# Optimization experiments

Measured on AMD Instinct MI355X. Metric: run time of the kernel, lower is better.

The kernel has to match this reference:

```python
import jax, jax.numpy as jnp
import numpy as np

B, S, K, D = 128, 64, 10, 256
THR = -1.5


def setup_inputs() -> dict:
    key = jax.random.key(0)
    ks = jax.random.split(key, 9)
    si = 1.0 / np.sqrt(D)  # torch GRU init: U(-1/sqrt(hidden), 1/sqrt(hidden))
    u = lambda k, shape, s: jax.random.uniform(k, shape, jnp.float32, -s, s)
    return {
        "item_embs": jax.random.normal(ks[0], (B, S, K, D), jnp.float32),
        "user_embs": jax.random.normal(ks[1], (B, S, D), jnp.float32),
        "W_ih": u(ks[2], (3 * D, 2 * D), si),
        "W_hh": u(ks[3], (3 * D, D), si),
        "b_ih": u(ks[4], (3 * D,), si),
        "b_hh": u(ks[5], (3 * D,), si),
        "w_out": u(ks[6], (D,), si),
        "b_out": u(ks[7], (), si),
        "length": jax.random.randint(ks[8], (B,), 0, S),
    }


def reference(item_embs, user_embs, W_ih, W_hh, b_ih, b_hh, w_out, b_out, length):
    N = B * S
    # x['items'] = cat([item_embs.flatten(0,1), zeros_like(...)], -1)  -> [N, K, 2D]
    items_flat = item_embs.reshape(N, K, D)
    items = jnp.concatenate([items_flat, jnp.zeros_like(items_flat)], axis=-1)
    # user hidden state: gather user_embs at (length-1, clamped), repeat over S
    idx = jnp.clip(length - 1, 0, None)  # [B]
    u0 = user_embs[jnp.arange(B), idx]   # [B, D]
    h0 = jnp.repeat(u0, S, axis=0)       # [N, D]

    def gru_cell(x, h):
        gi = x @ W_ih.T + b_ih  # [N, 3D]
        gh = h @ W_hh.T + b_hh
        i_r, i_z, i_n = jnp.split(gi, 3, axis=-1)
        h_r, h_z, h_n = jnp.split(gh, 3, axis=-1)
        r = jax.nn.sigmoid(i_r + h_r)
        z = jax.nn.sigmoid(i_z + h_z)
        n = jnp.tanh(i_n + r * h_n)
        return (1.0 - z) * n + z * h

    def step(carry, x_t):
        h, mask = carry  # mask [N,1]: readout threshold gate for the click-half of input
        x = jnp.concatenate([x_t[:, :D], x_t[:, D:] * mask], axis=-1)
        h = gru_cell(x, h)
        y = h @ w_out + b_out  # [N]
        next_mask = (jax.lax.stop_gradient(y) > THR).astype(x_t.dtype)[:, None]
        return (h, next_mask), y

    xs = jnp.swapaxes(items, 0, 1)  # [K, N, 2D]
    init = (h0, jnp.ones((N, 1), item_embs.dtype))
    _, ys = jax.lax.scan(step, init, xs)  # ys [K, N]
    y = jnp.swapaxes(ys, 0, 1)  # [N, K]
    # self.w = 1, self.b = 0 -> identity calibration
    return y.reshape(B, S, K)
```

## Files before the change

kernel.cpp:

```cpp
#include <hip/hip_runtime.h>

#define BB 128
#define SS 64
#define KK 10
#define DD 256
#define NN (BB*SS)
#define ROWS 32
#define NBLK (NN/ROWS)
#define NT 1024

typedef __attribute__((ext_vector_type(8))) short short8;
typedef __attribute__((ext_vector_type(4))) float f32x4;

#define FRAG_ELEMS (48*8*64*8)

__device__ __forceinline__ unsigned short f2bf(float f){
  union { float f; unsigned u; } v; v.f = f;
  unsigned r = (v.u + 0x7FFFu + ((v.u >> 16) & 1u)) >> 16;
  return (unsigned short)r;
}

__global__ void prep_weights(const float* __restrict__ Wih,
                             const float* __restrict__ Whh,
                             unsigned short* __restrict__ fw){
  int id = blockIdx.x * 256 + threadIdx.x;
  int arr = (id >= FRAG_ELEMS);
  int r = arr ? (id - FRAG_ELEMS) : id;
  int j  = r & 7;
  int l  = (r >> 3) & 63;
  int tk = (r >> 9) & 7;
  int tn = r >> 12;
  int c  = tn * 16 + (l & 15);
  int d  = tk * 32 + ((l >> 4) << 3) + j;
  float v = arr ? Whh[c * 256 + d] : Wih[c * 512 + d];
  fw[id] = f2bf(v);
}

__global__ __launch_bounds__(NT, 4) void gru_main(
    const float* __restrict__ item, const float* __restrict__ user,
    const float* __restrict__ b_ih, const float* __restrict__ b_hh,
    const float* __restrict__ w_out, const float* __restrict__ b_out,
    const int* __restrict__ length, const unsigned short* __restrict__ ws,
    float* __restrict__ out)
{
  __shared__ unsigned short xfrag[2][2*8*64*8];
  __shared__ unsigned short hfrag[2][2*8*64*8];
  __shared__ float yp[3][16][2][4][4];

  const int tid  = threadIdx.x;
  const int lane = tid & 63;
  const int w    = tid >> 6;
  const int col  = lane & 15;
  const int q    = lane >> 4;
  const int nb   = blockIdx.x * ROWS;
  const int b    = nb / SS;

  const short8* fw1 = (const short8*)ws;
  const short8* fwh = fw1 + (FRAG_ELEMS/8);

  const int d    = w*16 + col;
  const float br_  = b_ih[d]       + b_hh[d];
  const float bz_  = b_ih[256 + d] + b_hh[256 + d];
  const float bin_ = b_ih[512 + d];
  const float bhn_ = b_hh[512 + d];
  const float wo_  = w_out[d];

  int idx = length[b] - 1; if (idx < 0) idx = 0;
  const float u0 = user[((size_t)b*SS + idx)*DD + d];
  float h[2][4];
  #pragma unroll
  for (int mt = 0; mt < 2; ++mt)
    #pragma unroll
    for (int reg = 0; reg < 4; ++reg)
      h[mt][reg] = u0;

  const int tkk = d >> 5;
  const int slb = ((d >> 3) & 3) * 16;
  const int dj  = d & 7;
  {
    unsigned short hb = f2bf(u0);
    #pragma unroll
    for (int mt = 0; mt < 2; ++mt)
      #pragma unroll
      for (int reg = 0; reg < 4; ++reg)
        hfrag[0][((mt*8 + tkk)*64 + slb + q*4 + reg)*8 + dj] = hb;
  }

  const int xrow = tid >> 5;
  const int xo   = tid & 31;
  const int xmt  = xrow >> 4;
  const int xtk  = xo >> 2;
  const int xsl  = (xo & 3)*16 + (xrow & 15);
  {
    const float4* p = (const float4*)(item + ((size_t)(nb + xrow)*KK + 0)*DD + xo*8);
    float4 a0 = p[0], a1 = p[1];
    unsigned short t[8];
    t[0]=f2bf(a0.x); t[1]=f2bf(a0.y); t[2]=f2bf(a0.z); t[3]=f2bf(a0.w);
    t[4]=f2bf(a1.x); t[5]=f2bf(a1.y); t[6]=f2bf(a1.z); t[7]=f2bf(a1.w);
    *(short8*)&xfrag[0][((xmt*8 + xtk)*64 + xsl)*8] = *(short8*)t;
  }
  __syncthreads();

  const float bout = b_out[0];

  for (int k = 0; k < KK; ++k){
    const int cb  = k & 1;
    const int nbf = cb ^ 1;

    f32x4 acc[2][4];
    #pragma unroll
    for (int mt = 0; mt < 2; ++mt)
      #pragma unroll
      for (int kd = 0; kd < 4; ++kd){
        f32x4 z4 = {0.f, 0.f, 0.f, 0.f};
        acc[mt][kd] = z4;
      }

    #pragma unroll 2
    for (int tk = 0; tk < 8; ++tk){
      short8 ax0 = *(const short8*)&xfrag[cb][((0*8 + tk)*64 + lane)*8];
      short8 ax1 = *(const short8*)&xfrag[cb][((1*8 + tk)*64 + lane)*8];
      short8 ah0 = *(const short8*)&hfrag[cb][((0*8 + tk)*64 + lane)*8];
      short8 ah1 = *(const short8*)&hfrag[cb][((1*8 + tk)*64 + lane)*8];
      short8 w1r = fw1[((w     )*8 + tk)*64 + lane];
      short8 w1z = fw1[((16 + w)*8 + tk)*64 + lane];
      short8 w1n = fw1[((32 + w)*8 + tk)*64 + lane];
      short8 whr = fwh[((w     )*8 + tk)*64 + lane];
      short8 whz = fwh[((16 + w)*8 + tk)*64 + lane];
      short8 whn = fwh[((32 + w)*8 + tk)*64 + lane];
      acc[0][0] = __builtin_amdgcn_mfma_f32_16x16x32_bf16(ax0, w1r, acc[0][0], 0, 0, 0);
      acc[0][0] = __builtin_amdgcn_mfma_f32_16x16x32_bf16(ah0, whr, acc[0][0], 0, 0, 0);
      acc[0][1] = __builtin_amdgcn_mfma_f32_16x16x32_bf16(ax0, w1z, acc[0][1], 0, 0, 0);
      acc[0][1] = __builtin_amdgcn_mfma_f32_16x16x32_bf16(ah0, whz, acc[0][1], 0, 0, 0);
      acc[0][2] = __builtin_amdgcn_mfma_f32_16x16x32_bf16(ax0, w1n, acc[0][2], 0, 0, 0);
      acc[0][3] = __builtin_amdgcn_mfma_f32_16x16x32_bf16(ah0, whn, acc[0][3], 0, 0, 0);
      acc[1][0] = __builtin_amdgcn_mfma_f32_16x16x32_bf16(ax1, w1r, acc[1][0], 0, 0, 0);
      acc[1][0] = __builtin_amdgcn_mfma_f32_16x16x32_bf16(ah1, whr, acc[1][0], 0, 0, 0);
      acc[1][1] = __builtin_amdgcn_mfma_f32_16x16x32_bf16(ax1, w1z, acc[1][1], 0, 0, 0);
      acc[1][1] = __builtin_amdgcn_mfma_f32_16x16x32_bf16(ah1, whz, acc[1][1], 0, 0, 0);
      acc[1][2] = __builtin_amdgcn_mfma_f32_16x16x32_bf16(ax1, w1n, acc[1][2], 0, 0, 0);
      acc[1][3] = __builtin_amdgcn_mfma_f32_16x16x32_bf16(ah1, whn, acc[1][3], 0, 0, 0);
    }

    float4 xn0, xn1;
    if (k < KK-1){
      const float4* p = (const float4*)(item + ((size_t)(nb + xrow)*KK + (k+1))*DD + xo*8);
      xn0 = p[0]; xn1 = p[1];
    }

    float ypl[2][4];
    #pragma unroll
    for (int mt = 0; mt < 2; ++mt)
      #pragma unroll
      for (int reg = 0; reg < 4; ++reg){
        float rp = acc[mt][0][reg] + br_;
        float zp = acc[mt][1][reg] + bz_;
        float r  = 1.f / (1.f + __expf(-rp));
        float z  = 1.f / (1.f + __expf(-zp));
        float np = acc[mt][2][reg] + bin_ + r*(acc[mt][3][reg] + bhn_);
        np = fminf(fmaxf(np, -30.f), 30.f);
        float e  = __expf(2.f*np);
        float n  = (e - 1.f) / (e + 1.f);
        float hv = (1.f - z)*n + z*h[mt][reg];
        h[mt][reg] = hv;
        ypl[mt][reg] = hv * wo_;
      }

    #pragma unroll
    for (int mt = 0; mt < 2; ++mt)
      #pragma unroll
      for (int reg = 0; reg < 4; ++reg){
        float p = ypl[mt][reg];
        p += __shfl_xor(p, 1);
        p += __shfl_xor(p, 2);
        p += __shfl_xor(p, 4);
        p += __shfl_xor(p, 8);
        if (col == 0) yp[k % 3][w][mt][q][reg] = p;
      }

    #pragma unroll
    for (int mt = 0; mt < 2; ++mt)
      #pragma unroll
      for (int reg = 0; reg < 4; ++reg)
        hfrag[nbf][((mt*8 + tkk)*64 + slb + q*4 + reg)*8 + dj] = f2bf(h[mt][reg]);

    if (k < KK-1){
      unsigned short t[8];
      t[0]=f2bf(xn0.x); t[1]=f2bf(xn0.y); t[2]=f2bf(xn0.z); t[3]=f2bf(xn0.w);
      t[4]=f2bf(xn1.x); t[5]=f2bf(xn1.y); t[6]=f2bf(xn1.z); t[7]=f2bf(xn1.w);
      *(short8*)&xfrag[nbf][((xmt*8 + xtk)*64 + xsl)*8] = *(short8*)t;
    }

    if (k > 0 && tid < 32){
      float s = bout;
      #pragma unroll
      for (int ww = 0; ww < 16; ++ww)
        s += yp[(k-1) % 3][ww][tid >> 4][(tid >> 2) & 3][tid & 3];
      out[(size_t)(nb + tid)*KK + (k-1)] = s;
    }

    __syncthreads();
  }

  if (tid < 32){
    float s = bout;
    #pragma unroll
    for (int ww = 0; ww < 16; ++ww)
      s += yp[(KK-1) % 3][ww][tid >> 4][(tid >> 2) & 3][tid & 3];
    out[(size_t)(nb + tid)*KK + (KK-1)] = s;
  }
}

extern "C" void kernel_launch(void* const* d_in, const int* in_sizes, int n_in,
                              void* d_out, int out_size, void* d_ws, size_t ws_size,
                              hipStream_t stream) {
  const float* item   = (const float*)d_in[0];
  const float* user   = (const float*)d_in[1];
  const float* W_ih   = (const float*)d_in[2];
  const float* W_hh   = (const float*)d_in[3];
  const float* b_ih   = (const float*)d_in[4];
  const float* b_hh   = (const float*)d_in[5];
  const float* w_out  = (const float*)d_in[6];
  const float* b_out  = (const float*)d_in[7];
  const int*   length = (const int*)d_in[8];
  unsigned short* ws  = (unsigned short*)d_ws;
  float* out = (float*)d_out;

  hipLaunchKernelGGL(prep_weights, dim3((2*FRAG_ELEMS)/256), dim3(256), 0, stream,
                     W_ih, W_hh, ws);
  hipLaunchKernelGGL(gru_main, dim3(NBLK), dim3(NT), 0, stream,
                     item, user, b_ih, b_hh, w_out, b_out, length, ws, out);
}
```

Before: 232.7 us.

## Software-pipeline weight fragment loads with block-staggered K order and fast gate math

```diff
diff --git a/kernel.cpp b/kernel.cpp
--- a/kernel.cpp
+++ b/kernel.cpp
@@ -54,6 +54,7 @@
   const int q    = lane >> 4;
   const int nb   = blockIdx.x * ROWS;
   const int b    = nb / SS;
+  const int sk   = blockIdx.x & 7;
 
   const short8* fw1 = (const short8*)ws;
   const short8* fwh = fw1 + (FRAG_ELEMS/8);
@@ -64,6 +65,10 @@
   const float bin_ = b_ih[512 + d];
   const float bhn_ = b_hh[512 + d];
   const float wo_  = w_out[d];
+
+  const int wq0 = (w     )*512 + lane;
+  const int wq1 = (16 + w)*512 + lane;
+  const int wq2 = (32 + w)*512 + lane;
 
   int idx = length[b] - 1; if (idx < 0) idx = 0;
   const float u0 = user[((size_t)b*SS + idx)*DD + d];
@@ -99,9 +104,34 @@
     t[4]=f2bf(a1.x); t[5]=f2bf(a1.y); t[6]=f2bf(a1.z); t[7]=f2bf(a1.w);
     *(short8*)&xfrag[0][((xmt*8 + xtk)*64 + xsl)*8] = *(short8*)t;
   }
+
+  short8 wa0,wa1,wa2,wa3,wa4,wa5, wb0,wb1,wb2,wb3,wb4,wb5;
+  {
+    const int o_ = sk*64;
+    wa0 = fw1[wq0+o_]; wa1 = fw1[wq1+o_]; wa2 = fw1[wq2+o_];
+    wa3 = fwh[wq0+o_]; wa4 = fwh[wq1+o_]; wa5 = fwh[wq2+o_];
+  }
+
   __syncthreads();
 
   const float bout = b_out[0];
+
+#define MFMA16(A,Bv,C) __builtin_amdgcn_mfma_f32_16x16x32_bf16(A,Bv,C,0,0,0)
+#define TKSTEP(C0,C1,C2,C3,C4,C5, N0,N1,N2,N3,N4,N5, TK) do{ \
+      const int tkv_ = ((TK)+sk)&7; const int o_ = (((TK)+1+sk)&7)*64; \
+      N0 = fw1[wq0+o_]; N1 = fw1[wq1+o_]; N2 = fw1[wq2+o_]; \
+      N3 = fwh[wq0+o_]; N4 = fwh[wq1+o_]; N5 = fwh[wq2+o_]; \
+      short8 ax0 = *(const short8*)&xfrag[cb][((    tkv_)*64 + lane)*8]; \
+      short8 ax1 = *(const short8*)&xfrag[cb][((8 + tkv_)*64 + lane)*8]; \
+      short8 ah0 = *(const short8*)&hfrag[cb][((    tkv_)*64 + lane)*8]; \
+      short8 ah1 = *(const short8*)&hfrag[cb][((8 + tkv_)*64 + lane)*8]; \
+      acc[0][0] = MFMA16(ax0,C0,acc[0][0]); acc[0][0] = MFMA16(ah0,C3,acc[0][0]); \
+      acc[0][1] = MFMA16(ax0,C1,acc[0][1]); acc[0][1] = MFMA16(ah0,C4,acc[0][1]); \
+      acc[0][2] = MFMA16(ax0,C2,acc[0][2]); acc[0][3] = MFMA16(ah0,C5,acc[0][3]); \
+      acc[1][0] = MFMA16(ax1,C0,acc[1][0]); acc[1][0] = MFMA16(ah1,C3,acc[1][0]); \
+      acc[1][1] = MFMA16(ax1,C1,acc[1][1]); acc[1][1] = MFMA16(ah1,C4,acc[1][1]); \
+      acc[1][2] = MFMA16(ax1,C2,acc[1][2]); acc[1][3] = MFMA16(ah1,C5,acc[1][3]); \
+    }while(0)
 
   for (int k = 0; k < KK; ++k){
     const int cb  = k & 1;
@@ -115,32 +145,6 @@
         f32x4 z4 = {0.f, 0.f, 0.f, 0.f};
         acc[mt][kd] = z4;
       }
-
-    #pragma unroll 2
-    for (int tk = 0; tk < 8; ++tk){
-      short8 ax0 = *(const short8*)&xfrag[cb][((0*8 + tk)*64 + lane)*8];
-      short8 ax1 = *(const short8*)&xfrag[cb][((1*8 + tk)*64 + lane)*8];
-      short8 ah0 = *(const short8*)&hfrag[cb][((0*8 + tk)*64 + lane)*8];
-      short8 ah1 = *(const short8*)&hfrag[cb][((1*8 + tk)*64 + lane)*8];
-      short8 w1r = fw1[((w     )*8 + tk)*64 + lane];
-      short8 w1z = fw1[((16 + w)*8 + tk)*64 + lane];
-      short8 w1n = fw1[((32 + w)*8 + tk)*64 + lane];
-      short8 whr = fwh[((w     )*8 + tk)*64 + lane];
-      short8 whz = fwh[((16 + w)*8 + tk)*64 + lane];
-      short8 whn = fwh[((32 + w)*8 + tk)*64 + lane];
-      acc[0][0] = __builtin_amdgcn_mfma_f32_16x16x32_bf16(ax0, w1r, acc[0][0], 0, 0, 0);
-      acc[0][0] = __builtin_amdgcn_mfma_f32_16x16x32_bf16(ah0, whr, acc[0][0], 0, 0, 0);
-      acc[0][1] = __builtin_amdgcn_mfma_f32_16x16x32_bf16(ax0, w1z, acc[0][1], 0, 0, 0);
-      acc[0][1] = __builtin_amdgcn_mfma_f32_16x16x32_bf16(ah0, whz, acc[0][1], 0, 0, 0);
-      acc[0][2] = __builtin_amdgcn_mfma_f32_16x16x32_bf16(ax0, w1n, acc[0][2], 0, 0, 0);
-      acc[0][3] = __builtin_amdgcn_mfma_f32_16x16x32_bf16(ah0, whn, acc[0][3], 0, 0, 0);
-      acc[1][0] = __builtin_amdgcn_mfma_f32_16x16x32_bf16(ax1, w1r, acc[1][0], 0, 0, 0);
-      acc[1][0] = __builtin_amdgcn_mfma_f32_16x16x32_bf16(ah1, whr, acc[1][0], 0, 0, 0);
-      acc[1][1] = __builtin_amdgcn_mfma_f32_16x16x32_bf16(ax1, w1z, acc[1][1], 0, 0, 0);
-      acc[1][1] = __builtin_amdgcn_mfma_f32_16x16x32_bf16(ah1, whz, acc[1][1], 0, 0, 0);
-      acc[1][2] = __builtin_amdgcn_mfma_f32_16x16x32_bf16(ax1, w1n, acc[1][2], 0, 0, 0);
-      acc[1][3] = __builtin_amdgcn_mfma_f32_16x16x32_bf16(ah1, whn, acc[1][3], 0, 0, 0);
-    }
 
     float4 xn0, xn1;
     if (k < KK-1){
@@ -148,6 +152,15 @@
       xn0 = p[0]; xn1 = p[1];
     }
 
+    TKSTEP(wa0,wa1,wa2,wa3,wa4,wa5, wb0,wb1,wb2,wb3,wb4,wb5, 0);
+    TKSTEP(wb0,wb1,wb2,wb3,wb4,wb5, wa0,wa1,wa2,wa3,wa4,wa5, 1);
+    TKSTEP(wa0,wa1,wa2,wa3,wa4,wa5, wb0,wb1,wb2,wb3,wb4,wb5, 2);
+    TKSTEP(wb0,wb1,wb2,wb3,wb4,wb5, wa0,wa1,wa2,wa3,wa4,wa5, 3);
+    TKSTEP(wa0,wa1,wa2,wa3,wa4,wa5, wb0,wb1,wb2,wb3,wb4,wb5, 4);
+    TKSTEP(wb0,wb1,wb2,wb3,wb4,wb5, wa0,wa1,wa2,wa3,wa4,wa5, 5);
+    TKSTEP(wa0,wa1,wa2,wa3,wa4,wa5, wb0,wb1,wb2,wb3,wb4,wb5, 6);
+    TKSTEP(wb0,wb1,wb2,wb3,wb4,wb5, wa0,wa1,wa2,wa3,wa4,wa5, 7);
+
     float ypl[2][4];
     #pragma unroll
     for (int mt = 0; mt < 2; ++mt)
@@ -155,12 +168,12 @@
       for (int reg = 0; reg < 4; ++reg){
         float rp = acc[mt][0][reg] + br_;
         float zp = acc[mt][1][reg] + bz_;
-        float r  = 1.f / (1.f + __expf(-rp));
-        float z  = 1.f / (1.f + __expf(-zp));
+        float r  = __builtin_amdgcn_rcpf(1.f + __expf(-rp));
+        float z  = __builtin_amdgcn_rcpf(1.f + __expf(-zp));
         float np = acc[mt][2][reg] + bin_ + r*(acc[mt][3][reg] + bhn_);
-        np = fminf(fmaxf(np, -30.f), 30.f);
+        np = __builtin_amdgcn_fmed3f(np, -30.f, 30.f);
         float e  = __expf(2.f*np);
-        float n  = (e - 1.f) / (e + 1.f);
+        float n  = 1.f - 2.f*__builtin_amdgcn_rcpf(e + 1.f);
         float hv = (1.f - z)*n + z*h[mt][reg];
         h[mt][reg] = hv;
         ypl[mt][reg] = hv * wo_;
```

New measurement: 564.4 us. +142.5%, slower.
